# Kernel optimization log

Measured on AMD Instinct MI355X. Metric: run time of the kernel, lower is better.

Reference implementation:

```python
import jax, jax.numpy as jnp
import numpy as np
from jax import lax

B, T, U, H, INNER, V = 4, 200, 100, 320, 512, 1000
BLANK = 0


def setup_inputs() -> dict:
    key = jax.random.key(0)
    ks = jax.random.split(key, 8)
    enc_state = jax.random.normal(ks[0], (B, T, H), dtype=jnp.float32)
    dec_state = jax.random.normal(ks[1], (B, U + 1, H), dtype=jnp.float32)
    tokens = jax.random.randint(ks[2], (B, U), 1, V, dtype=jnp.int32)
    output_length = jnp.full((B,), T, dtype=jnp.int32)
    tokens_length = jnp.full((B,), U, dtype=jnp.int32)
    s1 = 1.0 / np.sqrt(2 * H)
    s2 = 1.0 / np.sqrt(INNER)
    W1 = jax.random.uniform(ks[3], (2 * H, INNER), minval=-s1, maxval=s1, dtype=jnp.float32)
    b1 = jax.random.uniform(ks[4], (INNER,), minval=-s1, maxval=s1, dtype=jnp.float32)
    W2 = jax.random.uniform(ks[5], (INNER, V), minval=-s2, maxval=s2, dtype=jnp.float32)
    b2 = jax.random.uniform(ks[6], (V,), minval=-s2, maxval=s2, dtype=jnp.float32)
    return {"enc_state": enc_state, "dec_state": dec_state, "tokens": tokens,
            "output_length": output_length, "tokens_length": tokens_length,
            "W1": W1, "b1": b1, "W2": W2, "b2": b2}


def joint_logits(enc_state, dec_state, W1, b1, W2, b2):
    # concat joint: cat(enc[b,t], dec[b,u]) @ W1 == enc @ W1[:H] + dec @ W1[H:]
    h_enc = jnp.einsum('bth,hi->bti', enc_state, W1[:H])      # (B,T,INNER)
    h_dec = jnp.einsum('buh,hi->bui', dec_state, W1[H:])      # (B,U+1,INNER)
    h = jnp.tanh(h_enc[:, :, None, :] + h_dec[:, None, :, :] + b1)  # (B,T,U+1,INNER)
    return jnp.einsum('btui,iv->btuv', h, W2) + b2            # (B,T,U+1,V)


def rnnt_loss(log_probs, tokens, output_length, tokens_length):
    # log_probs: (B,T,U+1,V); tokens: (B,U) int
    Bn, Tn, U1, _ = log_probs.shape
    blank_lp = log_probs[..., BLANK]                           # (B,T,U+1)
    label_lp = jnp.take_along_axis(
        log_probs[:, :, :U1 - 1, :],
        tokens[:, None, :, None].astype(jnp.int32).repeat(Tn, axis=1),
        axis=-1)[..., 0]                                       # (B,T,U)

    # row t=0: alpha[0,u] = sum_{u'<u} label_lp[0,u']
    def row0_step(c, a):
        n = c + a
        return n, n
    init0 = jnp.zeros((Bn,), dtype=log_probs.dtype)
    _, rest0 = lax.scan(row0_step, init0, label_lp[:, 0, :].T)  # (U,B)
    alpha0 = jnp.concatenate([init0[None], rest0], axis=0).T    # (B,U+1)

    def t_step(alpha_prev, xs):
        blank_prev, label_t = xs                # (B,U+1), (B,U)
        b = alpha_prev + blank_prev             # blank transition from row t-1
        def u_step(c, inp):
            b_u, a_prev = inp
            n = jnp.logaddexp(b_u, c + a_prev)
            return n, n
        first = b[:, 0]
        _, rest = lax.scan(u_step, first, (b[:, 1:].T, label_t.T))
        alpha_t = jnp.concatenate([first[None], rest], axis=0).T
        return alpha_t, alpha_t

    xs = (blank_lp[:, :-1, :].transpose(1, 0, 2), label_lp[:, 1:, :].transpose(1, 0, 2))
    _, alphas = lax.scan(t_step, alpha0, xs)                    # (T-1,B,U+1)
    alpha = jnp.concatenate([alpha0[None], alphas], axis=0).transpose(1, 0, 2)  # (B,T,U+1)

    bidx = jnp.arange(Bn)
    t_idx = output_length - 1
    u_idx = tokens_length
    ll = alpha[bidx, t_idx, u_idx] + blank_lp[bidx, t_idx, u_idx]
    return -jnp.mean(ll)


def reference(enc_state, dec_state, tokens, output_length, tokens_length, W1, b1, W2, b2):
    logits = joint_logits(enc_state, dec_state, W1, b1, W2, b2)
    log_probs = jax.nn.log_softmax(logits, axis=-1)
    return rnnt_loss(log_probs, tokens, output_length, tokens_length)
```

## Files before the change

kernel.cpp:

```cpp
#include <hip/hip_runtime.h>
#include <hip/hip_bf16.h>

#define T_DIM 200
#define U_DIM 100
#define U1    101
#define H_DIM 320
#define K_INNER 512
#define V_DIM 1000
#define B_DIM 4
#define ND 300
#define ROWS 48
#define XPITCH 520
#define CHUNK 8

typedef unsigned short ushort_t;
typedef unsigned char uchar_t;
typedef unsigned int uint32;
typedef long lfrag;

typedef float ffrag4 __attribute__((ext_vector_type(4)));

#define LOG2E   1.4426950408889634f
#define LOG2E16 (1.4426950408889634f * 0.0625f)
#define LN2     0.6931471805599453f

__device__ __forceinline__ float tanh_fast(float x) {
  float e = __expf(2.0f * x);
  return 1.0f - __fdividef(2.0f, e + 1.0f);
}

__device__ __forceinline__ uint2 pk_fp8x8(float t0, float t1, float t2, float t3,
                                          float t4, float t5, float t6, float t7) {
  uint2 r;
  r.x = (uint32)__builtin_amdgcn_cvt_pk_fp8_f32(t0, t1, 0, false);
  r.x = (uint32)__builtin_amdgcn_cvt_pk_fp8_f32(t2, t3, (int)r.x, true);
  r.y = (uint32)__builtin_amdgcn_cvt_pk_fp8_f32(t4, t5, 0, false);
  r.y = (uint32)__builtin_amdgcn_cvt_pk_fp8_f32(t6, t7, (int)r.y, true);
  return r;
}

__device__ __forceinline__ float dpp_up1(float v, float oldv) {
  return __int_as_float(__builtin_amdgcn_update_dpp(
      __float_as_int(oldv), __float_as_int(v), 0x138, 0xf, 0xf, false));
}

__global__ __launch_bounds__(512)
void prep_kernel(const float* __restrict__ enc, const float* __restrict__ dec,
                 const float* __restrict__ W1, const float* __restrict__ W2,
                 float* __restrict__ hEnc, float* __restrict__ hDec,
                 uchar_t* __restrict__ W2f8)
{
  __shared__ union { float sIn[8][H_DIM]; float sW[8][1024]; } sh;
  const int tid = threadIdx.x;
  const int blk = blockIdx.x;

  if (blk < 151) {
    const float* inp; float* outp; int nRows, rowOff, b0;
    if (blk < 100) { inp = enc; outp = hEnc; nRows = B_DIM * T_DIM; rowOff = 0;     b0 = blk; }
    else           { inp = dec; outp = hDec; nRows = B_DIM * U1;    rowOff = H_DIM; b0 = blk - 100; }
    const int r0 = b0 * 8;
    for (int i = tid; i < 8 * H_DIM; i += 512) {
      int r = i / H_DIM, k = i - r * H_DIM;
      int rr = r0 + r;
      sh.sIn[r][k] = (rr < nRows) ? inp[(size_t)rr * H_DIM + k] : 0.0f;
    }
    __syncthreads();
    const int c = tid;
    float acc[8];
#pragma unroll
    for (int r = 0; r < 8; ++r) acc[r] = 0.0f;
    const float* Wp = W1 + (size_t)rowOff * K_INNER + c;
    for (int k = 0; k < H_DIM; k += 4) {
      float w0 = Wp[(size_t)(k + 0) * K_INNER];
      float w1 = Wp[(size_t)(k + 1) * K_INNER];
      float w2 = Wp[(size_t)(k + 2) * K_INNER];
      float w3 = Wp[(size_t)(k + 3) * K_INNER];
#pragma unroll
      for (int r = 0; r < 8; ++r) {
        float4 s = *(const float4*)&sh.sIn[r][k];
        acc[r] = fmaf(s.w, w3, fmaf(s.z, w2, fmaf(s.y, w1, fmaf(s.x, w0, acc[r]))));
      }
    }
#pragma unroll
    for (int r = 0; r < 8; ++r) {
      int rr = r0 + r;
      if (rr < nRows) outp[(size_t)rr * K_INNER + c] = acc[r];
    }
  } else {
    const int kc = blk - 151;
    for (int i = tid; i < 8 * 1024; i += 512) {
      int r = i >> 10, n = i & 1023;
      sh.sW[r][n] = (n < V_DIM) ? W2[(size_t)(kc * 8 + r) * V_DIM + n] : 0.0f;
    }
    __syncthreads();
#pragma unroll
    for (int h = 0; h < 2; ++h) {
      int n = tid + h * 512;
      uint2 pk = pk_fp8x8(sh.sW[0][n] * 16.f, sh.sW[1][n] * 16.f,
                          sh.sW[2][n] * 16.f, sh.sW[3][n] * 16.f,
                          sh.sW[4][n] * 16.f, sh.sW[5][n] * 16.f,
                          sh.sW[6][n] * 16.f, sh.sW[7][n] * 16.f);
      *(uint2*)&W2f8[((size_t)kc * 1024 + n) * 8] = pk;
    }
  }
}

__global__ __launch_bounds__(256, 3)
void joint_kernel(const float* __restrict__ hEnc, const float* __restrict__ hDec,
                  const float* __restrict__ b1, const uchar_t* __restrict__ W2f8,
                  const float* __restrict__ b2, const int* __restrict__ tokens,
                  float* __restrict__ pD)
{
  __shared__ union SU {
    uchar_t X[ROWS * XPITCH];
    float red[4][ROWS][4];
  } sh;

  const int tid = threadIdx.x;
  const int b  = blockIdx.z;
  const int t0 = blockIdx.y * 12;
  const int u0 = blockIdx.x * 4;

  for (int i = tid; i < ROWS * 64; i += 256) {
    const int row = i >> 6;
    const int G = i & 63;
    const int tcl = min(t0 + (row >> 2), T_DIM - 1);
    const int ucl = min(u0 + (row & 3), U1 - 1);
    const float* er = hEnc + (size_t)(b * T_DIM + tcl) * K_INNER;
    const float* dr = hDec + (size_t)(b * U1 + ucl) * K_INNER;
    const int k = G << 3;
    float4 e0 = *(const float4*)(er + k);
    float4 e1 = *(const float4*)(er + k + 4);
    float4 d0 = *(const float4*)(dr + k);
    float4 d1 = *(const float4*)(dr + k + 4);
    float4 c0 = *(const float4*)(b1 + k);
    float4 c1 = *(const float4*)(b1 + k + 4);
    uint2 pk = pk_fp8x8(tanh_fast(e0.x + d0.x + c0.x), tanh_fast(e0.y + d0.y + c0.y),
                        tanh_fast(e0.z + d0.z + c0.z), tanh_fast(e0.w + d0.w + c0.w),
                        tanh_fast(e1.x + d1.x + c1.x), tanh_fast(e1.y + d1.y + c1.y),
                        tanh_fast(e1.z + d1.z + c1.z), tanh_fast(e1.w + d1.w + c1.w));
    *(uint2*)&sh.X[row * XPITCH + (G << 3)] = pk;
  }
  __syncthreads();

  const int wave = tid >> 6;
  const int lane = tid & 63;
  const int l15 = lane & 15;
  const int quad = lane >> 4;

  float sumexp[3][4], labelA[3][4], blankV[3][4];
#pragma unroll
  for (int i = 0; i < 3; ++i)
#pragma unroll
    for (int j = 0; j < 4; ++j) { sumexp[i][j] = 0.0f; labelA[i][j] = 0.0f; blankV[i][j] = 0.0f; }

  int tokv[4];
#pragma unroll
  for (int j = 0; j < 4; ++j)
    tokv[j] = (u0 + j < U_DIM) ? tokens[b * U_DIM + u0 + j] : -1;

  const uchar_t* aB = &sh.X[l15 * XPITCH + quad * 8];

#pragma unroll 1
  for (int ct = 0; ct < 4; ++ct) {
    const int nbase = ct * 256 + wave * 64;
    ffrag4 acc[3][4];
    ffrag4 zero4 = {0.0f, 0.0f, 0.0f, 0.0f};
#pragma unroll
    for (int rb = 0; rb < 3; ++rb)
#pragma unroll
      for (int cb = 0; cb < 4; ++cb) acc[rb][cb] = zero4;

    const uchar_t* bp = W2f8 + ((size_t)quad * 1024 + nbase + l15) * 8;

#pragma unroll 4
    for (int ks = 0; ks < 16; ++ks) {
      lfrag av[3];
#pragma unroll
      for (int rb = 0; rb < 3; ++rb)
        av[rb] = *(const lfrag*)(aB + rb * (16 * XPITCH) + ks * 32);
      lfrag bv[4];
#pragma unroll
      for (int cb = 0; cb < 4; ++cb)
        bv[cb] = *(const lfrag*)(bp + cb * 128);
      bp += 4 * 1024 * 8;
#pragma unroll
      for (int rb = 0; rb < 3; ++rb)
#pragma unroll
        for (int cb = 0; cb < 4; ++cb)
          acc[rb][cb] = __builtin_amdgcn_mfma_f32_16x16x32_fp8_fp8(av[rb], bv[cb], acc[rb][cb], 0, 0, 0);
    }

#pragma unroll
    for (int cb = 0; cb < 4; ++cb) {
      const int v = nbase + cb * 16 + l15;
      const float b2v = (v < V_DIM) ? b2[v] : -1e30f;
      const float b2s = b2v * LOG2E;
#pragma unroll
      for (int rb = 0; rb < 3; ++rb)
#pragma unroll
        for (int reg = 0; reg < 4; ++reg) {
          float a = acc[rb][cb][reg];
          sumexp[rb][reg] += exp2f(fmaf(a, LOG2E16, b2s));
          labelA[rb][reg] += (v == tokv[reg]) ? a : 0.0f;
        }
    }
    if (nbase == 0) {
#pragma unroll
      for (int rb = 0; rb < 3; ++rb)
#pragma unroll
        for (int reg = 0; reg < 4; ++reg) blankV[rb][reg] = acc[rb][0][reg];
    }
  }

#pragma unroll
  for (int mask = 1; mask <= 8; mask <<= 1) {
#pragma unroll
    for (int rb = 0; rb < 3; ++rb)
#pragma unroll
      for (int reg = 0; reg < 4; ++reg) {
        sumexp[rb][reg] += __shfl_xor(sumexp[rb][reg], mask, 64);
        labelA[rb][reg] += __shfl_xor(labelA[rb][reg], mask, 64);
      }
  }

  __syncthreads();
  if (l15 == 0) {
#pragma unroll
    for (int rb = 0; rb < 3; ++rb)
#pragma unroll
      for (int reg = 0; reg < 4; ++reg) {
        int row = rb * 16 + quad * 4 + reg;
        sh.red[wave][row][0] = sumexp[rb][reg];
        sh.red[wave][row][1] = blankV[rb][reg];
        sh.red[wave][row][2] = labelA[rb][reg];
      }
  }
  __syncthreads();
  if (tid < ROWS) {
    float S  = sh.red[0][tid][0] + sh.red[1][tid][0] + sh.red[2][tid][0] + sh.red[3][tid][0];
    float Bl = sh.red[0][tid][1] + sh.red[1][tid][1] + sh.red[2][tid][1] + sh.red[3][tid][1];
    float Lb = sh.red[0][tid][2] + sh.red[1][tid][2] + sh.red[2][tid][2] + sh.red[3][tid][2];
    int t = t0 + (tid >> 2);
    int u = u0 + (tid & 3);
    if (t < T_DIM && u < U1) {
      float lse2 = __log2f(S);
      int tok = (u < U_DIM) ? tokens[b * U_DIM + u] : 0;
      int d = t + u;
      size_t idx = (((size_t)b * ND + d) * 128 + u) * 2;
      pD[idx]     = fmaf(Bl, LOG2E16, b2[0]   * LOG2E) - lse2;
      pD[idx + 1] = fmaf(Lb, LOG2E16, b2[tok] * LOG2E) - lse2;
    }
  }
}

__global__ __launch_bounds__(256)
void dp_kernel(const float* __restrict__ pD,
               const int* __restrict__ outLen, const int* __restrict__ tokLen,
               float* __restrict__ outLoss)
{
  __shared__ float sD[4][3][CHUNK * 256];
  __shared__ float llsh[B_DIM];
  const int tid = threadIdx.x;
  const int wv = tid >> 6;
  const int lane = tid & 63;
  const float* src = pD + (size_t)wv * ND * 256;
  const int tIdx = outLen[wv] - 1;
  const int uIdx = tokLen[wv];
  const int dStar = tIdx + uIdx;
  const float NEG = -1e30f;
  const float blkStar = src[((size_t)dStar * 128 + uIdx) * 2];

  float aE = (lane == 0) ? 0.0f : NEG;
  float aO = NEG;
  float ll2 = 0.0f;
  if (dStar == 0 && lane == 0) ll2 = blkStar;

  const int uE = 2 * lane;

#define ISSUE(c, buf)                                                         \
  {                                                                           \
    const float* g_ = src + (size_t)(c) * (CHUNK * 256);                      \
    float* l_ = &sD[wv][(buf)][0];                                            \
    _Pragma("unroll")                                                         \
    for (int j_ = 0; j_ < CHUNK; ++j_)                                        \
      __builtin_amdgcn_global_load_lds(                                       \
        (const __attribute__((address_space(1))) void*)(g_ + j_ * 256 + lane * 4), \
        (__attribute__((address_space(3))) void*)(l_ + j_ * 256), 16, 0, 0);  \
  }

  ISSUE(0, 0)
  ISSUE(1, 1)
#pragma unroll 1
  for (int c = 0; c < 38; ++c) {
    { const int nc = c + 2; const int cc = nc <= 37 ? nc : 37; ISSUE(cc, nc % 3) }
    asm volatile("s_waitcnt vmcnt(16)" ::: "memory");
    const float* buf = &sD[wv][c % 3][0];
#pragma unroll
    for (int j = 0; j < CHUNK; ++j) {
      const int d = c * CHUNK + 1 + j;
      float4 q = *(const float4*)&buf[j * 256 + uE * 2];
      float aO_up = dpp_up1(aO, NEG);
      float labUp = dpp_up1(q.w, NEG);
      float bt0 = aE + q.x, lt0 = aO_up + labUp;
      float mx0 = fmaxf(bt0, lt0), mn0 = fminf(bt0, lt0);
      float r0 = mx0 + __log2f(1.0f + exp2f(mn0 - mx0));
      int te = d - uE;
      float nE = ((uE <= U_DIM) && (te >= 0) && (te < T_DIM)) ? r0 : NEG;
      float bt1 = aO + q.z, lt1 = aE + q.y;
      float mx1 = fmaxf(bt1, lt1), mn1 = fminf(bt1, lt1);
      float r1 = mx1 + __log2f(1.0f + exp2f(mn1 - mx1));
      int to = te - 1;
      float nO = ((uE + 1 <= U_DIM) && (to >= 0) && (to < T_DIM)) ? r1 : NEG;
      aE = nE; aO = nO;
      if (d == dStar) {
        if (uIdx == uE)          ll2 = nE + blkStar;
        else if (uIdx == uE + 1) ll2 = nO + blkStar;
      }
    }
  }
#undef ISSUE

#pragma unroll
  for (int mask = 1; mask < 64; mask <<= 1) ll2 += __shfl_xor(ll2, mask, 64);
  if (lane == 0) llsh[wv] = ll2;
  __syncthreads();
  if (tid == 0)
    outLoss[0] = -(llsh[0] + llsh[1] + llsh[2] + llsh[3]) * 0.25f * LN2;
}

extern "C" void kernel_launch(void* const* d_in, const int* in_sizes, int n_in,
                              void* d_out, int out_size, void* d_ws, size_t ws_size,
                              hipStream_t stream)
{
  const float* enc    = (const float*)d_in[0];
  const float* dec    = (const float*)d_in[1];
  const int*   tokens = (const int*)d_in[2];
  const int*   outLen = (const int*)d_in[3];
  const int*   tokLen = (const int*)d_in[4];
  const float* W1     = (const float*)d_in[5];
  const float* b1     = (const float*)d_in[6];
  const float* W2     = (const float*)d_in[7];
  const float* b2     = (const float*)d_in[8];
  float* out = (float*)d_out;

  char* ws = (char*)d_ws;
  float*   hEnc = (float*)(ws + 0);
  float*   hDec = (float*)(ws + 1638400);
  uchar_t* W2f8 = (uchar_t*)(ws + 2465792);
  float*   pD   = (float*)(ws + 2990080);

  prep_kernel<<<dim3(215), dim3(512), 0, stream>>>(enc, dec, W1, W2, hEnc, hDec, W2f8);
  joint_kernel<<<dim3(26, 17, B_DIM), dim3(256), 0, stream>>>(hEnc, hDec, b1, W2f8, b2, tokens, pD);
  dp_kernel<<<dim3(1), dim3(256), 0, stream>>>(pD, outLen, tokLen, out);
}
```

Before: 265.8 us.

## Stage fp8 W2 tiles through LDS with double-buffered async loads

Result: faster. 257.9 us (-3.0%).

```diff
diff --git a/kernel.cpp b/kernel.cpp
--- a/kernel.cpp
+++ b/kernel.cpp
@@ -93,6 +93,7 @@
       sh.sW[r][n] = (n < V_DIM) ? W2[(size_t)(kc * 8 + r) * V_DIM + n] : 0.0f;
     }
     __syncthreads();
+    const int ks = kc >> 2, q = kc & 3;
 #pragma unroll
     for (int h = 0; h < 2; ++h) {
       int n = tid + h * 512;
@@ -100,7 +101,9 @@
                           sh.sW[2][n] * 16.f, sh.sW[3][n] * 16.f,
                           sh.sW[4][n] * 16.f, sh.sW[5][n] * 16.f,
                           sh.sW[6][n] * 16.f, sh.sW[7][n] * 16.f);
-      *(uint2*)&W2f8[((size_t)kc * 1024 + n) * 8] = pk;
+      const int ct = n >> 8, w = (n >> 6) & 3, col = n & 63;
+      const size_t off = (size_t)(ct * 16 + ks) * 8192 + w * 2048 + q * 512 + col * 8;
+      *(uint2*)&W2f8[off] = pk;
     }
   }
 }
@@ -115,11 +118,29 @@
     uchar_t X[ROWS * XPITCH];
     float red[4][ROWS][4];
   } sh;
+  __shared__ __align__(16) uchar_t sB[4][2][2048];
 
   const int tid = threadIdx.x;
   const int b  = blockIdx.z;
   const int t0 = blockIdx.y * 12;
   const int u0 = blockIdx.x * 4;
+  const int wave = tid >> 6;
+  const int lane = tid & 63;
+  const int l15 = lane & 15;
+  const int quad = lane >> 4;
+
+  float b2s[4][4];
+#pragma unroll
+  for (int ct = 0; ct < 4; ++ct)
+#pragma unroll
+    for (int cb = 0; cb < 4; ++cb) {
+      int v = ct * 256 + wave * 64 + cb * 16 + l15;
+      b2s[ct][cb] = (v < V_DIM) ? b2[v] * LOG2E : -1e30f;
+    }
+  int tokv[4];
+#pragma unroll
+  for (int j = 0; j < 4; ++j)
+    tokv[j] = (u0 + j < U_DIM) ? tokens[b * U_DIM + u0 + j] : -1;
 
   for (int i = tid; i < ROWS * 64; i += 256) {
     const int row = i >> 6;
@@ -143,27 +164,33 @@
   }
   __syncthreads();
 
-  const int wave = tid >> 6;
-  const int lane = tid & 63;
-  const int l15 = lane & 15;
-  const int quad = lane >> 4;
+  uchar_t* sBw = &sB[wave][0][0];
+  const uchar_t* gW = W2f8 + (size_t)wave * 2048 + (size_t)lane * 16;
+
+#define STAGE(gbase, bufv)                                                          \
+  {                                                                                 \
+    __builtin_amdgcn_global_load_lds(                                               \
+        (const __attribute__((address_space(1))) void*)(gbase),                     \
+        (__attribute__((address_space(3))) void*)(sBw + (bufv) * 2048), 16, 0, 0);  \
+    __builtin_amdgcn_global_load_lds(                                               \
+        (const __attribute__((address_space(1))) void*)((gbase) + 1024),            \
+        (__attribute__((address_space(3))) void*)(sBw + (bufv) * 2048 + 1024), 16, 0, 0); \
+  }
+
+  STAGE(gW, 0)
+  const uchar_t* gP = gW + 8192;
+
+  const uchar_t* aB = &sh.X[l15 * XPITCH + quad * 8];
+  const uchar_t* bL = sBw + quad * 512 + l15 * 8;
 
   float sumexp[3][4], labelA[3][4], blankV[3][4];
 #pragma unroll
   for (int i = 0; i < 3; ++i)
 #pragma unroll
     for (int j = 0; j < 4; ++j) { sumexp[i][j] = 0.0f; labelA[i][j] = 0.0f; blankV[i][j] = 0.0f; }
-
-  int tokv[4];
-#pragma unroll
-  for (int j = 0; j < 4; ++j)
-    tokv[j] = (u0 + j < U_DIM) ? tokens[b * U_DIM + u0 + j] : -1;
-
-  const uchar_t* aB = &sh.X[l15 * XPITCH + quad * 8];
 
 #pragma unroll 1
   for (int ct = 0; ct < 4; ++ct) {
-    const int nbase = ct * 256 + wave * 64;
     ffrag4 acc[3][4];
     ffrag4 zero4 = {0.0f, 0.0f, 0.0f, 0.0f};
 #pragma unroll
@@ -171,10 +198,15 @@
 #pragma unroll
       for (int cb = 0; cb < 4; ++cb) acc[rb][cb] = zero4;
 
-    const uchar_t* bp = W2f8 + ((size_t)quad * 1024 + nbase + l15) * 8;
-
-#pragma unroll 4
+#pragma unroll
     for (int ks = 0; ks < 16; ++ks) {
+      if (ks < 15 || ct < 3) {
+        STAGE(gP, (ks + 1) & 1)
+        gP += 8192;
+        asm volatile("s_waitcnt vmcnt(2)" ::: "memory");
+      } else {
+        asm volatile("s_waitcnt vmcnt(0)" ::: "memory");
+      }
       lfrag av[3];
 #pragma unroll
       for (int rb = 0; rb < 3; ++rb)
@@ -182,8 +214,7 @@
       lfrag bv[4];
 #pragma unroll
       for (int cb = 0; cb < 4; ++cb)
-        bv[cb] = *(const lfrag*)(bp + cb * 128);
-      bp += 4 * 1024 * 8;
+        bv[cb] = *(const lfrag*)(bL + (ks & 1) * 2048 + cb * 128);
 #pragma unroll
       for (int rb = 0; rb < 3; ++rb)
 #pragma unroll
@@ -193,25 +224,25 @@
 
 #pragma unroll
     for (int cb = 0; cb < 4; ++cb) {
-      const int v = nbase + cb * 16 + l15;
-      const float b2v = (v < V_DIM) ? b2[v] : -1e30f;
-      const float b2s = b2v * LOG2E;
+      const int v = ct * 256 + wave * 64 + cb * 16 + l15;
+      const float bs = b2s[ct][cb];
 #pragma unroll
       for (int rb = 0; rb < 3; ++rb)
 #pragma unroll
         for (int reg = 0; reg < 4; ++reg) {
           float a = acc[rb][cb][reg];
-          sumexp[rb][reg] += exp2f(fmaf(a, LOG2E16, b2s));
+          sumexp[rb][reg] += exp2f(fmaf(a, LOG2E16, bs));
           labelA[rb][reg] += (v == tokv[reg]) ? a : 0.0f;
         }
     }
-    if (nbase == 0) {
+    if (ct == 0 && wave == 0) {
 #pragma unroll
       for (int rb = 0; rb < 3; ++rb)
 #pragma unroll
         for (int reg = 0; reg < 4; ++reg) blankV[rb][reg] = acc[rb][0][reg];
     }
   }
+#undef STAGE
 
 #pragma unroll
   for (int mask = 1; mask <= 8; mask <<= 1) {
@@ -259,7 +290,7 @@
                const int* __restrict__ outLen, const int* __restrict__ tokLen,
                float* __restrict__ outLoss)
 {
-  __shared__ float sD[4][3][CHUNK * 256];
+  __shared__ __align__(16) float sD[4][3][CHUNK * 256];
   __shared__ float llsh[B_DIM];
   const int tid = threadIdx.x;
   const int wv = tid >> 6;
@@ -296,10 +327,14 @@
     { const int nc = c + 2; const int cc = nc <= 37 ? nc : 37; ISSUE(cc, nc % 3) }
     asm volatile("s_waitcnt vmcnt(16)" ::: "memory");
     const float* buf = &sD[wv][c % 3][0];
+    float4 qv[CHUNK];
+#pragma unroll
+    for (int j = 0; j < CHUNK; ++j)
+      qv[j] = *(const float4*)&buf[j * 256 + uE * 2];
 #pragma unroll
     for (int j = 0; j < CHUNK; ++j) {
       const int d = c * CHUNK + 1 + j;
-      float4 q = *(const float4*)&buf[j * 256 + uE * 2];
+      float4 q = qv[j];
       float aO_up = dpp_up1(aO, NEG);
       float labUp = dpp_up1(q.w, NEG);
       float bt0 = aE + q.x, lt0 = aO_up + labUp;
```
